# Performance work log

Hardware: AMD Instinct MI355X
Metric: run time of the kernel (lower is better)

Reference implementation:

```python
import jax, jax.numpy as jnp
from jax import lax
import numpy as np

NUM_LAYERS = 4
NUM_HEADS = 4
FUTURE_FRAMES = 2
EPS = 1e-5  # torch default for BatchNorm1d and LayerNorm


def setup_inputs() -> dict:
    key = jax.random.key(0)
    ks = jax.random.split(key, 8)
    B, F, T, C2, BC = 1024, 257, 3, 3, 32
    IN_DIM = T * C2 * 2  # 18
    L, H = NUM_LAYERS, NUM_HEADS
    s = 0.1
    inp = {
        "x": jax.random.normal(ks[0], (B, F, T, C2, 2), dtype=jnp.float32),
        "in_w": jax.random.normal(ks[1], (IN_DIM, BC), dtype=jnp.float32) * s,
        "in_b": jnp.zeros((BC,), jnp.float32),
        "conv_w": jax.random.normal(ks[2], (L, 3, BC, BC), dtype=jnp.float32) * s,  # (L, W, Cin, Cout)
        "bn_g": jnp.ones((L, BC), jnp.float32),
        "bn_b": jnp.zeros((L, BC), jnp.float32),
        "qkv_w": jax.random.normal(ks[3], (L, BC, 3 * BC), dtype=jnp.float32) * s,
        "proj_w": jax.random.normal(ks[4], (L, BC, BC), dtype=jnp.float32) * s,
        "proj_b": jnp.zeros((L, BC), jnp.float32),
        "ln_g": jnp.ones((L, BC), jnp.float32),
        "ln_b": jnp.zeros((L, BC), jnp.float32),
        "h1_w": jax.random.normal(ks[5], (BC, BC // 2), dtype=jnp.float32) * s,
        "h1_b": jnp.zeros((BC // 2,), jnp.float32),
        "h2_w": jax.random.normal(ks[6], (BC // 2, 1), dtype=jnp.float32) * s,
        "h2_b": jnp.zeros((1,), jnp.float32),
    }
    return inp


def _banded_attention(x, qkv_w, proj_w, proj_b):
    # x: (B, F, C); window = [i, i + FUTURE_FRAMES]
    B, F, C = x.shape
    H, D = NUM_HEADS, C // NUM_HEADS
    qkv = x @ qkv_w                                   # (B, F, 3C)
    q, k, v = jnp.split(qkv, 3, axis=-1)
    q = q.reshape(B, F, H, D)
    k = k.reshape(B, F, H, D)
    v = v.reshape(B, F, H, D)
    scores = jnp.einsum("bihd,bjhd->bhij", q, k) * (D ** -0.5)
    i = jnp.arange(F)[:, None]
    j = jnp.arange(F)[None, :]
    allowed = (j >= i) & (j <= i + FUTURE_FRAMES)     # width-3 band
    scores = jnp.where(allowed, scores, -jnp.inf)
    attn = jax.nn.softmax(scores, axis=-1)
    out = jnp.einsum("bhij,bjhd->bihd", attn, v).reshape(B, F, C)
    return out @ proj_w + proj_b


def _layer(x, cw, bg, bb, qw, pw, pb, lg, lb):
    # conv over freq axis, channels-last: (B, F, C)
    c = lax.conv_general_dilated(x, cw, window_strides=(1,), padding="SAME",
                                 dimension_numbers=("NWC", "WIO", "NWC"))
    # BatchNorm1d in training mode: stats over (batch, freq), biased variance
    mu = c.mean(axis=(0, 1))
    var = c.var(axis=(0, 1))
    c = (c - mu) * lax.rsqrt(var + EPS) * bg + bb
    c = jax.nn.gelu(c, approximate=False)             # nn.GELU exact
    y = c + _banded_attention(x, qw, pw, pb)
    m = y.mean(axis=-1, keepdims=True)
    v = y.var(axis=-1, keepdims=True)
    return (y - m) * lax.rsqrt(v + EPS) * lg + lb


def reference(x, in_w, in_b, conv_w, bn_g, bn_b, qkv_w, proj_w, proj_b,
              ln_g, ln_b, h1_w, h1_b, h2_w, h2_b):
    B, F = x.shape[0], x.shape[1]
    h = x.reshape(B, F, -1) @ in_w + in_b             # (B, F, 32)
    for l in range(NUM_LAYERS):
        h = _layer(h, conv_w[l], bn_g[l], bn_b[l], qkv_w[l],
                   proj_w[l], proj_b[l], ln_g[l], ln_b[l])
    s = jax.nn.gelu(h @ h1_w + h1_b, approximate=False)
    mask = jax.nn.sigmoid(s @ h2_w + h2_b)            # (B, F, 1)
    return mask
```

## Files before the change

kernel.cpp:

```cpp
#include <hip/hip_runtime.h>
#include <math.h>


#define BB 1024
#define FF 257
#define BF (BB*FF)
#define TILE 64
#define NT 5
#define NBLK (BB*NT)
#define NLAYER 4
#define SQ 36

__device__ __forceinline__ float gelu_exact(float x){
    return 0.5f*x*(1.0f+erff(x*0.70710678118654752f));
}
__device__ __forceinline__ float dot4(float4 a, float4 b, float acc){
    return fmaf(a.x,b.x,fmaf(a.y,b.y,fmaf(a.z,b.z,fmaf(a.w,b.w,acc))));
}

__global__ __launch_bounds__(256) void k_zero(float* __restrict__ stats){
    stats[threadIdx.x]=0.0f;
}

__global__ __launch_bounds__(256) void k_inproj(const float* __restrict__ x,
        const float* __restrict__ in_w, const float* __restrict__ in_b,
        float* __restrict__ h)
{
    __shared__ float xs[TILE*18];
    int b = blockIdx.x / NT, t = blockIdx.x % NT, t0 = t*TILE;
    int tid = threadIdx.x;
    int nv = min(TILE, FF-t0);
    for (int i=tid;i<nv*18;i+=256) xs[i]=x[(size_t)(b*FF+t0)*18+i];
    __syncthreads();
    int co=tid&31, rq=tid>>5, rbase=rq*8;
    float bias = in_b[co];
    float a0=bias,a1=bias,a2=bias,a3=bias,a4=bias,a5=bias,a6=bias,a7=bias;
    #pragma unroll
    for (int ci=0;ci<18;ci++){
        float w = in_w[ci*32+co];
        a0=fmaf(xs[(rbase+0)*18+ci],w,a0);
        a1=fmaf(xs[(rbase+1)*18+ci],w,a1);
        a2=fmaf(xs[(rbase+2)*18+ci],w,a2);
        a3=fmaf(xs[(rbase+3)*18+ci],w,a3);
        a4=fmaf(xs[(rbase+4)*18+ci],w,a4);
        a5=fmaf(xs[(rbase+5)*18+ci],w,a5);
        a6=fmaf(xs[(rbase+6)*18+ci],w,a6);
        a7=fmaf(xs[(rbase+7)*18+ci],w,a7);
    }
    size_t base=(size_t)(b*FF+t0+rbase)*32+co;
    if (rbase+0<nv) h[base+0*32]=a0;
    if (rbase+1<nv) h[base+1*32]=a1;
    if (rbase+2<nv) h[base+2*32]=a2;
    if (rbase+3<nv) h[base+3*32]=a3;
    if (rbase+4<nv) h[base+4*32]=a4;
    if (rbase+5<nv) h[base+5*32]=a5;
    if (rbase+6<nv) h[base+6*32]=a6;
    if (rbase+7<nv) h[base+7*32]=a7;
}

#define CONV_C4_BODY(HSROW) \
    { float4 hv; \
      hv=*(const float4*)(HSROW+0*32); a0=dot4(hv,w0,a0); \
      hv=*(const float4*)(HSROW+1*32); a0=dot4(hv,w1,a0); a1=dot4(hv,w0,a1); \
      hv=*(const float4*)(HSROW+2*32); a0=dot4(hv,w2,a0); a1=dot4(hv,w1,a1); a2=dot4(hv,w0,a2); \
      hv=*(const float4*)(HSROW+3*32); a1=dot4(hv,w2,a1); a2=dot4(hv,w1,a2); a3=dot4(hv,w0,a3); \
      hv=*(const float4*)(HSROW+4*32); a2=dot4(hv,w2,a2); a3=dot4(hv,w1,a3); a4=dot4(hv,w0,a4); \
      hv=*(const float4*)(HSROW+5*32); a3=dot4(hv,w2,a3); a4=dot4(hv,w1,a4); a5=dot4(hv,w0,a5); \
      hv=*(const float4*)(HSROW+6*32); a4=dot4(hv,w2,a4); a5=dot4(hv,w1,a5); a6=dot4(hv,w0,a6); \
      hv=*(const float4*)(HSROW+7*32); a5=dot4(hv,w2,a5); a6=dot4(hv,w1,a6); a7=dot4(hv,w0,a7); \
      hv=*(const float4*)(HSROW+8*32); a6=dot4(hv,w2,a6); a7=dot4(hv,w1,a7); \
      hv=*(const float4*)(HSROW+9*32); a7=dot4(hv,w2,a7); }

__global__ __launch_bounds__(256) void k_convstats(const float* __restrict__ h,
        const float* __restrict__ conv_w, int layer, float* __restrict__ partials)
{
    __shared__ float hs[66*32];
    __shared__ float ps[8][32];
    __shared__ float pq[8][32];
    int b=blockIdx.x/NT, t=blockIdx.x%NT, t0=t*TILE, tid=threadIdx.x;
    for (int i4=tid;i4<66*8;i4+=256){
        int r=i4>>3, f=t0-1+r;
        float4 v=make_float4(0.f,0.f,0.f,0.f);
        if (f>=0 && f<FF) v=*(const float4*)(h+(size_t)(b*FF+f)*32+(i4&7)*4);
        *(float4*)&hs[r*32+(i4&7)*4]=v;
    }
    __syncthreads();
    int co=tid&31, rq=tid>>5, rbase=rq*8;
    const float* wl = conv_w + layer*3072 + co;
    float a0=0.f,a1=0.f,a2=0.f,a3=0.f,a4=0.f,a5=0.f,a6=0.f,a7=0.f;
    #pragma unroll 1
    for (int c4=0;c4<8;c4++){
        const float* w=wl+c4*128;
        float4 w0=make_float4(w[0],   w[32],  w[64],  w[96]);
        float4 w1=make_float4(w[1024],w[1056],w[1088],w[1120]);
        float4 w2=make_float4(w[2048],w[2080],w[2112],w[2144]);
        const float* hb=&hs[rbase*32+c4*4];
        CONV_C4_BODY(hb)
    }
    float ssum=0.f, ssq=0.f;
    if (t0+rbase+0<FF){ ssum+=a0; ssq+=a0*a0; }
    if (t0+rbase+1<FF){ ssum+=a1; ssq+=a1*a1; }
    if (t0+rbase+2<FF){ ssum+=a2; ssq+=a2*a2; }
    if (t0+rbase+3<FF){ ssum+=a3; ssq+=a3*a3; }
    if (t0+rbase+4<FF){ ssum+=a4; ssq+=a4*a4; }
    if (t0+rbase+5<FF){ ssum+=a5; ssq+=a5*a5; }
    if (t0+rbase+6<FF){ ssum+=a6; ssq+=a6*a6; }
    if (t0+rbase+7<FF){ ssum+=a7; ssq+=a7*a7; }
    ps[rq][co]=ssum; pq[rq][co]=ssq;
    __syncthreads();
    if (tid<32){
        float s=0.f;
        #pragma unroll
        for(int q=0;q<8;q++) s+=ps[q][tid];
        partials[blockIdx.x*64+tid]=s;
    } else if (tid<64){
        int cc=tid-32;
        float s=0.f;
        #pragma unroll
        for(int q=0;q<8;q++) s+=pq[q][cc];
        partials[blockIdx.x*64+tid]=s;
    }
}

__global__ __launch_bounds__(256) void k_reduce(const float* __restrict__ partials,
        float* __restrict__ stats)
{
    __shared__ float sm[4][64];
    int tid=threadIdx.x, col=tid&63, rq=tid>>6;
    int r0=blockIdx.x*80;
    float s=0.f;
    for (int k=rq;k<80;k+=4) s += partials[(r0+k)*64+col];
    sm[rq][col]=s;
    __syncthreads();
    if (tid<64){
        float v=sm[0][tid]+sm[1][tid]+sm[2][tid]+sm[3][tid];
        atomicAdd(&stats[tid], v);
    }
}

#define LN_STORE(Y,K) { \
    float s=(Y); \
    s+=__shfl_xor(s,1); s+=__shfl_xor(s,2); s+=__shfl_xor(s,4); \
    s+=__shfl_xor(s,8); s+=__shfl_xor(s,16); \
    float m=s*(1.0f/32.0f); \
    float dd=(Y)-m; float v=dd*dd; \
    v+=__shfl_xor(v,1); v+=__shfl_xor(v,2); v+=__shfl_xor(v,4); \
    v+=__shfl_xor(v,8); v+=__shfl_xor(v,16); \
    float rsd=rsqrtf(v*(1.0f/32.0f)+1e-5f); \
    if (t0+rbase+(K)<FF) hn[(size_t)(b*FF+t0+rbase+(K))*32+co]=dd*rsd*lgv+lbv; }

__global__ __launch_bounds__(256) void k_layer(const float* __restrict__ h,
        float* __restrict__ hn, const float* __restrict__ stats,
        const float* __restrict__ conv_w, const float* __restrict__ bn_g,
        const float* __restrict__ bn_b, const float* __restrict__ qkv_w,
        const float* __restrict__ proj_w, const float* __restrict__ proj_b,
        const float* __restrict__ ln_g, const float* __restrict__ ln_b, int layer)
{
    __shared__ float hs[67*32];
    __shared__ float qs[66*SQ];
    __shared__ float ks[66*SQ];
    __shared__ float vs[66*SQ];

    int b=blockIdx.x/NT, t=blockIdx.x%NT, t0=t*TILE, tid=threadIdx.x;
    for (int i4=tid;i4<67*8;i4+=256){
        int r=i4>>3, f=t0-1+r;
        float4 v=make_float4(0.f,0.f,0.f,0.f);
        if (f>=0 && f<FF) v=*(const float4*)(h+(size_t)(b*FF+f)*32+(i4&7)*4);
        *(float4*)&hs[r*32+(i4&7)*4]=v;
    }
    __syncthreads();

    if (tid<192){
        int j=tid%96, g=tid/96;
        const float* qwp = qkv_w + layer*3072 + j;
        float4 wv0=make_float4(qwp[0*96], qwp[1*96], qwp[2*96], qwp[3*96]);
        float4 wv1=make_float4(qwp[4*96], qwp[5*96], qwp[6*96], qwp[7*96]);
        float4 wv2=make_float4(qwp[8*96], qwp[9*96], qwp[10*96],qwp[11*96]);
        float4 wv3=make_float4(qwp[12*96],qwp[13*96],qwp[14*96],qwp[15*96]);
        float4 wv4=make_float4(qwp[16*96],qwp[17*96],qwp[18*96],qwp[19*96]);
        float4 wv5=make_float4(qwp[20*96],qwp[21*96],qwp[22*96],qwp[23*96]);
        float4 wv6=make_float4(qwp[24*96],qwp[25*96],qwp[26*96],qwp[27*96]);
        float4 wv7=make_float4(qwp[28*96],qwp[29*96],qwp[30*96],qwp[31*96]);
        int cbase = (j<32)? j : ((j<64)? j-32 : j-64);
        float* dst = (j<32)? qs : ((j<64)? ks : vs);
        #pragma unroll 1
        for (int rr=0;rr<33;rr++){
            int r=g*33+rr;
            if (t0+r<FF){
                const float* hr=&hs[(r+1)*32];
                float acc;
                acc=dot4(*(const float4*)(hr+ 0),wv0,0.f);
                acc=dot4(*(const float4*)(hr+ 4),wv1,acc);
                acc=dot4(*(const float4*)(hr+ 8),wv2,acc);
                acc=dot4(*(const float4*)(hr+12),wv3,acc);
                acc=dot4(*(const float4*)(hr+16),wv4,acc);
                acc=dot4(*(const float4*)(hr+20),wv5,acc);
                acc=dot4(*(const float4*)(hr+24),wv6,acc);
                acc=dot4(*(const float4*)(hr+28),wv7,acc);
                dst[r*SQ+cbase]=acc;
            }
        }
    }
    int co=tid&31, rq=tid>>5, rbase=rq*8;
    float y0,y1,y2,y3,y4,y5,y6,y7;
    {
        float mu  = stats[co]*(1.0f/(float)BF);
        float var = stats[32+co]*(1.0f/(float)BF) - mu*mu;
        float rs  = rsqrtf(fmaxf(var,0.f)+1e-5f);
        float g   = bn_g[layer*32+co];
        float scv = g*rs;
        float shv = bn_b[layer*32+co] - mu*g*rs;
        const float* wl = conv_w + layer*3072 + co;
        float a0=0.f,a1=0.f,a2=0.f,a3=0.f,a4=0.f,a5=0.f,a6=0.f,a7=0.f;
        #pragma unroll 1
        for (int c4=0;c4<8;c4++){
            const float* w=wl+c4*128;
            float4 w0=make_float4(w[0],   w[32],  w[64],  w[96]);
            float4 w1=make_float4(w[1024],w[1056],w[1088],w[1120]);
            float4 w2=make_float4(w[2048],w[2080],w[2112],w[2144]);
            const float* hb=&hs[rbase*32+c4*4];
            CONV_C4_BODY(hb)
        }
        y0=gelu_exact(fmaf(a0,scv,shv));
        y1=gelu_exact(fmaf(a1,scv,shv));
        y2=gelu_exact(fmaf(a2,scv,shv));
        y3=gelu_exact(fmaf(a3,scv,shv));
        y4=gelu_exact(fmaf(a4,scv,shv));
        y5=gelu_exact(fmaf(a5,scv,shv));
        y6=gelu_exact(fmaf(a6,scv,shv));
        y7=gelu_exact(fmaf(a7,scv,shv));
    }
    __syncthreads();

    {
        int r=tid>>2, hh=tid&3, f=t0+r;
        if (f<FF){
            int base=hh*8;
            float4 qa=*(const float4*)&qs[r*SQ+base];
            float4 qb=*(const float4*)&qs[r*SQ+base+4];
            float s0, s1=-1e30f, s2=-1e30f;
            s0=dot4(qa,*(const float4*)&ks[r*SQ+base],
               dot4(qb,*(const float4*)&ks[r*SQ+base+4],0.f))*0.35355339059327373f;
            if (f+1<FF)
                s1=dot4(qa,*(const float4*)&ks[(r+1)*SQ+base],
                   dot4(qb,*(const float4*)&ks[(r+1)*SQ+base+4],0.f))*0.35355339059327373f;
            if (f+2<FF)
                s2=dot4(qa,*(const float4*)&ks[(r+2)*SQ+base],
                   dot4(qb,*(const float4*)&ks[(r+2)*SQ+base+4],0.f))*0.35355339059327373f;
            float mx=fmaxf(s0,fmaxf(s1,s2));
            float e0=expf(s0-mx);
            float e1=(f+1<FF)?expf(s1-mx):0.f;
            float e2=(f+2<FF)?expf(s2-mx):0.f;
            float inv=1.0f/(e0+e1+e2);
            float4 va=*(const float4*)&vs[r*SQ+base];
            float4 vb=*(const float4*)&vs[r*SQ+base+4];
            float4 oa=make_float4(e0*va.x,e0*va.y,e0*va.z,e0*va.w);
            float4 ob=make_float4(e0*vb.x,e0*vb.y,e0*vb.z,e0*vb.w);
            if (f+1<FF){
                va=*(const float4*)&vs[(r+1)*SQ+base];
                vb=*(const float4*)&vs[(r+1)*SQ+base+4];
                oa.x=fmaf(e1,va.x,oa.x); oa.y=fmaf(e1,va.y,oa.y);
                oa.z=fmaf(e1,va.z,oa.z); oa.w=fmaf(e1,va.w,oa.w);
                ob.x=fmaf(e1,vb.x,ob.x); ob.y=fmaf(e1,vb.y,ob.y);
                ob.z=fmaf(e1,vb.z,ob.z); ob.w=fmaf(e1,vb.w,ob.w);
            }
            if (f+2<FF){
                va=*(const float4*)&vs[(r+2)*SQ+base];
                vb=*(const float4*)&vs[(r+2)*SQ+base+4];
                oa.x=fmaf(e2,va.x,oa.x); oa.y=fmaf(e2,va.y,oa.y);
                oa.z=fmaf(e2,va.z,oa.z); oa.w=fmaf(e2,va.w,oa.w);
                ob.x=fmaf(e2,vb.x,ob.x); ob.y=fmaf(e2,vb.y,ob.y);
                ob.z=fmaf(e2,vb.z,ob.z); ob.w=fmaf(e2,vb.w,ob.w);
            }
            oa.x*=inv; oa.y*=inv; oa.z*=inv; oa.w*=inv;
            ob.x*=inv; ob.y*=inv; ob.z*=inv; ob.w*=inv;
            *(float4*)&qs[r*SQ+base]=oa;
            *(float4*)&qs[r*SQ+base+4]=ob;
        }
    }
    __syncthreads();

    {
        const float* pwl = proj_w + layer*1024 + co;
        float pbv = proj_b[layer*32+co];
        float d0=pbv,d1=pbv,d2=pbv,d3=pbv,d4=pbv,d5=pbv,d6=pbv,d7=pbv;
        #pragma unroll 1
        for (int c4=0;c4<8;c4++){
            const float* w=pwl+c4*128;
            float4 wv=make_float4(w[0],w[32],w[64],w[96]);
            const float* qb=&qs[rbase*SQ+c4*4];
            d0=dot4(*(const float4*)(qb+0*SQ),wv,d0);
            d1=dot4(*(const float4*)(qb+1*SQ),wv,d1);
            d2=dot4(*(const float4*)(qb+2*SQ),wv,d2);
            d3=dot4(*(const float4*)(qb+3*SQ),wv,d3);
            d4=dot4(*(const float4*)(qb+4*SQ),wv,d4);
            d5=dot4(*(const float4*)(qb+5*SQ),wv,d5);
            d6=dot4(*(const float4*)(qb+6*SQ),wv,d6);
            d7=dot4(*(const float4*)(qb+7*SQ),wv,d7);
        }
        y0+=d0; y1+=d1; y2+=d2; y3+=d3; y4+=d4; y5+=d5; y6+=d6; y7+=d7;
    }

    {
        float lgv=ln_g[layer*32+co];
        float lbv=ln_b[layer*32+co];
        LN_STORE(y0,0) LN_STORE(y1,1) LN_STORE(y2,2) LN_STORE(y3,3)
        LN_STORE(y4,4) LN_STORE(y5,5) LN_STORE(y6,6) LN_STORE(y7,7)
    }
}

__global__ __launch_bounds__(256) void k_head(const float* __restrict__ h,
        const float* __restrict__ h1_w, const float* __restrict__ h1_b,
        const float* __restrict__ h2_w, const float* __restrict__ h2_b,
        float* __restrict__ out)
{
    __shared__ float hs[256*SQ];
    __shared__ float w1t[16*32];
    int tid=threadIdx.x;
    int r0=blockIdx.x*256;
    for (int i4=tid;i4<256*8;i4+=256){
        float4 v=*(const float4*)(h+(size_t)r0*32+i4*4);
        *(float4*)&hs[(i4>>3)*SQ+(i4&7)*4]=v;
    }
    for (int i=tid;i<512;i+=256) w1t[i]=h1_w[(i&31)*16+(i>>5)];
    __syncthreads();
    float4 hv0=*(const float4*)&hs[tid*SQ+ 0];
    float4 hv1=*(const float4*)&hs[tid*SQ+ 4];
    float4 hv2=*(const float4*)&hs[tid*SQ+ 8];
    float4 hv3=*(const float4*)&hs[tid*SQ+12];
    float4 hv4=*(const float4*)&hs[tid*SQ+16];
    float4 hv5=*(const float4*)&hs[tid*SQ+20];
    float4 hv6=*(const float4*)&hs[tid*SQ+24];
    float4 hv7=*(const float4*)&hs[tid*SQ+28];
    float acc2=h2_b[0];
    #pragma unroll
    for (int j=0;j<16;j++){
        const float* wr=&w1t[j*32];
        float aj=h1_b[j];
        aj=dot4(hv0,*(const float4*)(wr+ 0),aj);
        aj=dot4(hv1,*(const float4*)(wr+ 4),aj);
        aj=dot4(hv2,*(const float4*)(wr+ 8),aj);
        aj=dot4(hv3,*(const float4*)(wr+12),aj);
        aj=dot4(hv4,*(const float4*)(wr+16),aj);
        aj=dot4(hv5,*(const float4*)(wr+20),aj);
        aj=dot4(hv6,*(const float4*)(wr+24),aj);
        aj=dot4(hv7,*(const float4*)(wr+28),aj);
        acc2=fmaf(gelu_exact(aj), h2_w[j], acc2);
    }
    out[r0+tid]=1.0f/(1.0f+expf(-acc2));
}

extern "C" void kernel_launch(void* const* d_in, const int* in_sizes, int n_in,
                              void* d_out, int out_size, void* d_ws, size_t ws_size,
                              hipStream_t stream)
{
    const float* x     =(const float*)d_in[0];
    const float* in_w  =(const float*)d_in[1];
    const float* in_b  =(const float*)d_in[2];
    const float* conv_w=(const float*)d_in[3];
    const float* bn_g  =(const float*)d_in[4];
    const float* bn_b  =(const float*)d_in[5];
    const float* qkv_w =(const float*)d_in[6];
    const float* proj_w=(const float*)d_in[7];
    const float* proj_b=(const float*)d_in[8];
    const float* ln_g  =(const float*)d_in[9];
    const float* ln_b  =(const float*)d_in[10];
    const float* h1_w  =(const float*)d_in[11];
    const float* h1_b  =(const float*)d_in[12];
    const float* h2_w  =(const float*)d_in[13];
    const float* h2_b  =(const float*)d_in[14];

    float* bufA     = (float*)d_ws;
    float* bufB     = bufA + (size_t)BF*32;
    float* partials = bufB + (size_t)BF*32;
    float* stats    = partials + (size_t)NBLK*64;

    k_zero<<<1,256,0,stream>>>(stats);
    k_inproj<<<NBLK,256,0,stream>>>(x,in_w,in_b,bufA);
    for (int l=0;l<NLAYER;l++){
        float* cur = (l&1)? bufB : bufA;
        float* nxt = (l&1)? bufA : bufB;
        k_convstats<<<NBLK,256,0,stream>>>(cur, conv_w, l, partials);
        k_reduce<<<64,256,0,stream>>>(partials, stats + l*64);
        k_layer<<<NBLK,256,0,stream>>>(cur, nxt, stats+l*64, conv_w, bn_g, bn_b,
                                       qkv_w, proj_w, proj_b, ln_g, ln_b, l);
    }
    k_head<<<1028,256,0,stream>>>(bufA, h1_w,h1_b,h2_w,h2_b, (float*)d_out);
}
```

Measured before the change: 728.8 us.

## Fuse QKV projection into conv loop to reuse shared-memory row loads

```diff
diff --git a/kernel.cpp b/kernel.cpp
--- a/kernel.cpp
+++ b/kernel.cpp
@@ -170,37 +170,6 @@
     }
     __syncthreads();
 
-    if (tid<192){
-        int j=tid%96, g=tid/96;
-        const float* qwp = qkv_w + layer*3072 + j;
-        float4 wv0=make_float4(qwp[0*96], qwp[1*96], qwp[2*96], qwp[3*96]);
-        float4 wv1=make_float4(qwp[4*96], qwp[5*96], qwp[6*96], qwp[7*96]);
-        float4 wv2=make_float4(qwp[8*96], qwp[9*96], qwp[10*96],qwp[11*96]);
-        float4 wv3=make_float4(qwp[12*96],qwp[13*96],qwp[14*96],qwp[15*96]);
-        float4 wv4=make_float4(qwp[16*96],qwp[17*96],qwp[18*96],qwp[19*96]);
-        float4 wv5=make_float4(qwp[20*96],qwp[21*96],qwp[22*96],qwp[23*96]);
-        float4 wv6=make_float4(qwp[24*96],qwp[25*96],qwp[26*96],qwp[27*96]);
-        float4 wv7=make_float4(qwp[28*96],qwp[29*96],qwp[30*96],qwp[31*96]);
-        int cbase = (j<32)? j : ((j<64)? j-32 : j-64);
-        float* dst = (j<32)? qs : ((j<64)? ks : vs);
-        #pragma unroll 1
-        for (int rr=0;rr<33;rr++){
-            int r=g*33+rr;
-            if (t0+r<FF){
-                const float* hr=&hs[(r+1)*32];
-                float acc;
-                acc=dot4(*(const float4*)(hr+ 0),wv0,0.f);
-                acc=dot4(*(const float4*)(hr+ 4),wv1,acc);
-                acc=dot4(*(const float4*)(hr+ 8),wv2,acc);
-                acc=dot4(*(const float4*)(hr+12),wv3,acc);
-                acc=dot4(*(const float4*)(hr+16),wv4,acc);
-                acc=dot4(*(const float4*)(hr+20),wv5,acc);
-                acc=dot4(*(const float4*)(hr+24),wv6,acc);
-                acc=dot4(*(const float4*)(hr+28),wv7,acc);
-                dst[r*SQ+cbase]=acc;
-            }
-        }
-    }
     int co=tid&31, rq=tid>>5, rbase=rq*8;
     float y0,y1,y2,y3,y4,y5,y6,y7;
     {
@@ -210,16 +179,48 @@
         float g   = bn_g[layer*32+co];
         float scv = g*rs;
         float shv = bn_b[layer*32+co] - mu*g*rs;
-        const float* wl = conv_w + layer*3072 + co;
+        const float* wcl = conv_w + layer*3072 + co;
+        const float* wql = qkv_w + layer*3072 + co;
         float a0=0.f,a1=0.f,a2=0.f,a3=0.f,a4=0.f,a5=0.f,a6=0.f,a7=0.f;
+        float q0=0.f,q1=0.f,q2=0.f,q3=0.f,q4=0.f,q5=0.f,q6=0.f,q7=0.f;
+        float k0=0.f,k1=0.f,k2=0.f,k3=0.f,k4=0.f,k5=0.f,k6=0.f,k7=0.f;
+        float v0=0.f,v1=0.f,v2=0.f,v3=0.f,v4=0.f,v5=0.f,v6=0.f,v7=0.f;
+        float ek=0.f, ev=0.f;
+        int edge = (tid<64);
         #pragma unroll 1
         for (int c4=0;c4<8;c4++){
-            const float* w=wl+c4*128;
+            const float* w=wcl+c4*128;
             float4 w0=make_float4(w[0],   w[32],  w[64],  w[96]);
             float4 w1=make_float4(w[1024],w[1056],w[1088],w[1120]);
             float4 w2=make_float4(w[2048],w[2080],w[2112],w[2144]);
+            const float* qw=wql+c4*384;
+            float4 wq=make_float4(qw[0],  qw[96], qw[192],qw[288]);
+            float4 wk=make_float4(qw[32], qw[128],qw[224],qw[320]);
+            float4 wv=make_float4(qw[64], qw[160],qw[256],qw[352]);
             const float* hb=&hs[rbase*32+c4*4];
-            CONV_C4_BODY(hb)
+            float4 hv;
+            hv=*(const float4*)(hb+0*32); a0=dot4(hv,w0,a0);
+            hv=*(const float4*)(hb+1*32); a0=dot4(hv,w1,a0); a1=dot4(hv,w0,a1);
+                q0=dot4(hv,wq,q0); k0=dot4(hv,wk,k0); v0=dot4(hv,wv,v0);
+            hv=*(const float4*)(hb+2*32); a0=dot4(hv,w2,a0); a1=dot4(hv,w1,a1); a2=dot4(hv,w0,a2);
+                q1=dot4(hv,wq,q1); k1=dot4(hv,wk,k1); v1=dot4(hv,wv,v1);
+            hv=*(const float4*)(hb+3*32); a1=dot4(hv,w2,a1); a2=dot4(hv,w1,a2); a3=dot4(hv,w0,a3);
+                q2=dot4(hv,wq,q2); k2=dot4(hv,wk,k2); v2=dot4(hv,wv,v2);
+            hv=*(const float4*)(hb+4*32); a2=dot4(hv,w2,a2); a3=dot4(hv,w1,a3); a4=dot4(hv,w0,a4);
+                q3=dot4(hv,wq,q3); k3=dot4(hv,wk,k3); v3=dot4(hv,wv,v3);
+            hv=*(const float4*)(hb+5*32); a3=dot4(hv,w2,a3); a4=dot4(hv,w1,a4); a5=dot4(hv,w0,a5);
+                q4=dot4(hv,wq,q4); k4=dot4(hv,wk,k4); v4=dot4(hv,wv,v4);
+            hv=*(const float4*)(hb+6*32); a4=dot4(hv,w2,a4); a5=dot4(hv,w1,a5); a6=dot4(hv,w0,a6);
+                q5=dot4(hv,wq,q5); k5=dot4(hv,wk,k5); v5=dot4(hv,wv,v5);
+            hv=*(const float4*)(hb+7*32); a5=dot4(hv,w2,a5); a6=dot4(hv,w1,a6); a7=dot4(hv,w0,a7);
+                q6=dot4(hv,wq,q6); k6=dot4(hv,wk,k6); v6=dot4(hv,wv,v6);
+            hv=*(const float4*)(hb+8*32); a6=dot4(hv,w2,a6); a7=dot4(hv,w1,a7);
+                q7=dot4(hv,wq,q7); k7=dot4(hv,wk,k7); v7=dot4(hv,wv,v7);
+            hv=*(const float4*)(hb+9*32); a7=dot4(hv,w2,a7);
+            if (edge){
+                float4 he=*(const float4*)(&hs[(65+rq)*32+c4*4]);
+                ek=dot4(he,wk,ek); ev=dot4(he,wv,ev);
+            }
         }
         y0=gelu_exact(fmaf(a0,scv,shv));
         y1=gelu_exact(fmaf(a1,scv,shv));
@@ -229,6 +230,16 @@
         y5=gelu_exact(fmaf(a5,scv,shv));
         y6=gelu_exact(fmaf(a6,scv,shv));
         y7=gelu_exact(fmaf(a7,scv,shv));
+        int rb=rbase*SQ+co;
+        qs[rb+0*SQ]=q0; ks[rb+0*SQ]=k0; vs[rb+0*SQ]=v0;
+        qs[rb+1*SQ]=q1; ks[rb+1*SQ]=k1; vs[rb+1*SQ]=v1;
+        qs[rb+2*SQ]=q2; ks[rb+2*SQ]=k2; vs[rb+2*SQ]=v2;
+        qs[rb+3*SQ]=q3; ks[rb+3*SQ]=k3; vs[rb+3*SQ]=v3;
+        qs[rb+4*SQ]=q4; ks[rb+4*SQ]=k4; vs[rb+4*SQ]=v4;
+        qs[rb+5*SQ]=q5; ks[rb+5*SQ]=k5; vs[rb+5*SQ]=v5;
+        qs[rb+6*SQ]=q6; ks[rb+6*SQ]=k6; vs[rb+6*SQ]=v6;
+        qs[rb+7*SQ]=q7; ks[rb+7*SQ]=k7; vs[rb+7*SQ]=v7;
+        if (edge){ ks[(64+rq)*SQ+co]=ek; vs[(64+rq)*SQ+co]=ev; }
     }
     __syncthreads();
 
```

Measured after the change: 712.6 us. 1.02x faster.
